# Kernel optimization log

Measured on AMD Instinct MI355X. Metric: run time of the kernel, lower is better.

The kernel has to match this reference:

```python
import jax, jax.numpy as jnp
import numpy as np

NUM_HEADS = 8
KEY_DIM = 512      # total projected dim across heads
VALUE_DIM = 512
EMBED_DIM = 512


def setup_inputs() -> dict:
    key = jax.random.key(0)
    ks = jax.random.split(key, 12)
    B, S, E = 8, 1024, EMBED_DIM
    sc_in = 1.0 / np.sqrt(E)
    sc_o = 1.0 / np.sqrt(KEY_DIM)
    return {
        "queries": jax.random.normal(ks[0], (B, S, E), jnp.float32),
        "keys": jax.random.normal(ks[1], (B, S, E), jnp.float32),
        "values": jax.random.normal(ks[2], (B, S, E), jnp.float32),
        "Wq": jax.random.normal(ks[3], (E, KEY_DIM), jnp.float32) * sc_in,
        "bq": jnp.zeros((KEY_DIM,), jnp.float32),
        "Wk": jax.random.normal(ks[4], (E, KEY_DIM), jnp.float32) * sc_in,
        "bk": jnp.zeros((KEY_DIM,), jnp.float32),
        "Wv": jax.random.normal(ks[5], (E, VALUE_DIM), jnp.float32) * sc_in,
        "bv": jnp.zeros((VALUE_DIM,), jnp.float32),
        "Wo": jax.random.normal(ks[6], (KEY_DIM, EMBED_DIM), jnp.float32) * sc_o,
        "bo": jnp.zeros((EMBED_DIM,), jnp.float32),
    }


def _split_heads(x):
    # [B, S, key_dim] -> [B, H, S, key_dim//H]
    B, S, D = x.shape
    return x.reshape(B, S, NUM_HEADS, D // NUM_HEADS).transpose(0, 2, 1, 3)


def reference(queries, keys, values, Wq, bq, Wk, bk, Wv, bv, Wo, bo):
    q = _split_heads(queries @ Wq + bq)   # [B,H,S,dh]
    k = _split_heads(keys @ Wk + bk)
    v = _split_heads(values @ Wv + bv)
    # NOTE: original scales by sqrt(full key_dim), not per-head dim
    scores = jnp.einsum("bhqd,bhkd->bhqk", q, k) / jnp.sqrt(
        jnp.asarray(KEY_DIM, jnp.float32))
    weights = jax.nn.softmax(scores, axis=-1)
    o = jnp.einsum("bhqk,bhkd->bhqd", weights, v)  # [B,H,S,dh]
    B, H, S, dh = o.shape
    o = o.transpose(0, 2, 1, 3).reshape(B, S, H * dh)  # merge heads -> key_dim
    return o @ Wo + bo
```

## Files before the change

kernel.cpp:

```cpp
#include <hip/hip_runtime.h>


typedef __bf16 bf16x8 __attribute__((ext_vector_type(8)));
typedef __bf16 bf16x4 __attribute__((ext_vector_type(4)));
typedef float  f32x4  __attribute__((ext_vector_type(4)));

#define MFMA(a, b, c) __builtin_amdgcn_mfma_f32_16x16x32_bf16((a), (b), (c), 0, 0, 0)

#define WAITN_BAR(N) asm volatile("s_waitcnt vmcnt(" #N ")\n\ts_barrier" ::: "memory")

__device__ inline float fast_exp2(float x) {
  float r;
  asm("v_exp_f32 %0, %1" : "=v"(r) : "v"(x));
  return r;
}

__device__ inline bf16x8 cvt8(const float* p) {
  f32x4 u = *(const f32x4*)p;
  f32x4 v = *(const f32x4*)(p + 4);
  bf16x8 r;
  r[0] = (__bf16)u[0]; r[1] = (__bf16)u[1]; r[2] = (__bf16)u[2]; r[3] = (__bf16)u[3];
  r[4] = (__bf16)v[0]; r[5] = (__bf16)v[1]; r[6] = (__bf16)v[2]; r[7] = (__bf16)v[3];
  return r;
}

__device__ inline void gl_lds(const __bf16* g, __bf16* l) {
  __builtin_amdgcn_global_load_lds((const __attribute__((address_space(1))) void*)g,
                                   (__attribute__((address_space(3))) void*)l, 16, 0, 0);
}

__global__ __launch_bounds__(256) void prep(
    const float* __restrict__ Q, const float* __restrict__ K,
    const float* __restrict__ V, __bf16* __restrict__ Qo,
    __bf16* __restrict__ Ko, __bf16* __restrict__ Vo,
    const float* __restrict__ W0, const float* __restrict__ W1,
    const float* __restrict__ W2, const float* __restrict__ W3,
    __bf16* __restrict__ O0, __bf16* __restrict__ O1,
    __bf16* __restrict__ O2, __bf16* __restrict__ O3, float s0) {
  const int bx = blockIdx.x;
  if (bx < 2048) {
    const long idx = ((long)bx * 256 + threadIdx.x) * 8;
    *(bf16x8*)(Qo + idx) = cvt8(Q + idx);
    *(bf16x8*)(Ko + idx) = cvt8(K + idx);
    *(bf16x8*)(Vo + idx) = cvt8(V + idx);
    return;
  }
  const int bx2 = bx - 2048;
  const float* in;
  __bf16* out;
  float sc = 1.0f;
  switch (bx2 >> 6) {
    case 0: in = W0; out = O0; sc = s0; break;
    case 1: in = W1; out = O1; break;
    case 2: in = W2; out = O2; break;
    default: in = W3; out = O3; break;
  }
  const int ti = bx2 & 63;
  __shared__ __align__(16) float t[64][65];
  const int tk = (ti & 7) * 64;
  const int tn = (ti >> 3) * 64;
  const int r0 = threadIdx.x >> 4;
  const int c4 = threadIdx.x & 15;
#pragma unroll
  for (int i = 0; i < 4; ++i) {
    int r = r0 + i * 16;
    f32x4 v = *(const f32x4*)(in + (long)(tk + r) * 512 + tn + c4 * 4);
#pragma unroll
    for (int j = 0; j < 4; ++j) t[r][c4 * 4 + j] = v[j] * sc;
  }
  __syncthreads();
  const int n0 = threadIdx.x >> 3;
  const int k8 = threadIdx.x & 7;
#pragma unroll
  for (int i = 0; i < 2; ++i) {
    int n = n0 + i * 32;
    bf16x8 v;
#pragma unroll
    for (int j = 0; j < 8; ++j) v[j] = (__bf16)t[k8 * 8 + j][n];
    *(bf16x8*)(out + (long)(tn + n) * 512 + tk + k8 * 8) = v;
  }
}

template <int MODE, typename OT>
__device__ __forceinline__ void gemm_core(const __bf16* __restrict__ X,
                                          const __bf16* __restrict__ Wt,
                                          const float* __restrict__ bias,
                                          OT* __restrict__ out, float bsc,
                                          char* smem) {
  __bf16* At = (__bf16*)smem;
  __bf16* Bt = (__bf16*)(smem + 24576);

  const int tid = threadIdx.x;
  const int lane = tid & 63, wid = tid >> 6, quad = lane >> 4, l16 = lane & 15;
  const int i = blockIdx.x;
  const int kk = i >> 3;
  const int bm = ((i & 7) * 8 + (kk >> 2)) * 128;
  const int bn = (kk & 3) * 128;
  const int wm = (wid >> 1) * 64;
  const int wn = (wid & 1) * 64;

  f32x4 acc[4][4] = {};

  const int rowB = lane >> 2;
  const int gB = (lane & 3) ^ ((rowB >> 1) & 3);

  auto stage = [&](int off, int k0) {
#pragma unroll
    for (int j = 0; j < 2; ++j) {
      const int g = wid * 2 + j;
      gl_lds(X + (long)(bm + g * 16 + rowB) * 512 + k0 + (gB << 3),
             &At[off + g * 512 + lane * 8]);
      gl_lds(Wt + (long)(bn + g * 16 + rowB) * 512 + k0 + (gB << 3),
             &Bt[off + g * 512 + lane * 8]);
    }
  };

  const int posm = quad ^ ((l16 >> 1) & 3);

  auto compute = [&](int co) {
    bf16x8 a[4], b[4];
#pragma unroll
    for (int t = 0; t < 4; ++t) {
      a[t] = *(const bf16x8*)(&At[co + (wm + t * 16 + l16) * 32 + (posm << 3)]);
      b[t] = *(const bf16x8*)(&Bt[co + (wn + t * 16 + l16) * 32 + (posm << 3)]);
    }
#pragma unroll
    for (int mt = 0; mt < 4; ++mt)
#pragma unroll
      for (int nt = 0; nt < 4; ++nt) acc[mt][nt] = MFMA(a[mt], b[nt], acc[mt][nt]);
  };

  stage(0, 0);
  stage(4096, 32);

  int co = 0, so = 8192;
  for (int c = 0; c < 15; ++c) {
    WAITN_BAR(4);
    if (c < 14) stage(so, (c + 2) * 32);
    compute(co);
    const int nc = 12288 - co - so;
    so = co;
    co = nc;
  }
  WAITN_BAR(0);
  compute(co);

  if constexpr (MODE == 4) {
    __syncthreads();
    __bf16* tb = (__bf16*)smem;
#pragma unroll
    for (int nt = 0; nt < 4; ++nt) {
      const int n = wn + nt * 16 + l16;
      const float bvv = bias[bn + n] * bsc;
#pragma unroll
      for (int mt = 0; mt < 4; ++mt) {
        const int m0 = wm + mt * 16 + quad * 4;
        bf16x4 w;
#pragma unroll
        for (int r = 0; r < 4; ++r) w[r] = (__bf16)(acc[mt][nt][r] + bvv);
        *(bf16x4*)(&tb[n * 128 + (((m0 >> 3) ^ (n & 15)) << 3) + (m0 & 7)]) = w;
      }
    }
    __syncthreads();
    const int nn = tid & 127, mhalf = tid >> 7;
    const int h = (bn + nn) >> 6;
    const int bb = bm >> 10;
    OT* ob = out + (long)(bb * 8 + h) * 65536;
    const int cbase = (bm & 1023) >> 6;
#pragma unroll
    for (int gi = 0; gi < 8; ++gi) {
      const int gl = mhalf * 8 + gi;
      bf16x8 v = *(const bf16x8*)(&tb[nn * 128 + ((gl ^ (nn & 15)) << 3)]);
      const long idx = ((((long)(cbase + (gl >> 3)) * 4 + ((nn >> 4) & 3)) * 2 +
                        ((gl >> 2) & 1)) * 64 + (gl & 3) * 16 + (nn & 15)) * 8;
      *(bf16x8*)(ob + idx) = v;
    }
    return;
  }

#pragma unroll
  for (int nt = 0; nt < 4; ++nt) {
    const int n = bn + wn + nt * 16 + l16;
    const float bvv = bias[n] * bsc;
    const int h = n >> 6, d = n & 63;
#pragma unroll
    for (int mt = 0; mt < 4; ++mt) {
#pragma unroll
      for (int r = 0; r < 4; ++r) {
        const int m = bm + wm + mt * 16 + quad * 4 + r;
        const float v = acc[mt][nt][r] + bvv;
        if constexpr (MODE == 0) {
          out[(long)m * 512 + n] = (OT)v;
        } else if constexpr (MODE == 1) {
          const int bb = m >> 10, s = m & 1023;
          out[((long)((bb * 8 + h) * 1024 + s)) * 64 + d] = (OT)v;
        } else {
          const int bb = m >> 10, s = m & 1023;
          const long idx = (long)(bb * 8 + h) * 65536 +
                           ((((s >> 6) * 4 + ((s >> 4) & 3)) * 2 + (d >> 5)) * 64 +
                            ((d >> 3) & 3) * 16 + (s & 15)) * 8 + (d & 7);
          out[idx] = (OT)v;
        }
      }
    }
  }
}

__global__ __launch_bounds__(256) void gemm_qkv(
    const __bf16* __restrict__ Qx, const __bf16* __restrict__ Kx,
    const __bf16* __restrict__ Vx, const __bf16* __restrict__ Wqt,
    const __bf16* __restrict__ Wkt, const __bf16* __restrict__ Wvt,
    const float* __restrict__ bq, const float* __restrict__ bk,
    const float* __restrict__ bv, __bf16* __restrict__ Qp,
    __bf16* __restrict__ Kp, __bf16* __restrict__ Vtp, float qscale) {
  __shared__ __align__(16) char smem[49152];
  if (blockIdx.y == 0)
    gemm_core<1, __bf16>(Qx, Wqt, bq, Qp, qscale, smem);
  else if (blockIdx.y == 1)
    gemm_core<3, __bf16>(Kx, Wkt, bk, Kp, 1.0f, smem);
  else
    gemm_core<4, __bf16>(Vx, Wvt, bv, Vtp, 1.0f, smem);
}

__global__ __launch_bounds__(256) void gemm_o(const __bf16* __restrict__ Oc,
                                              const __bf16* __restrict__ Wot,
                                              const float* __restrict__ bo,
                                              float* __restrict__ out) {
  __shared__ __align__(16) char smem[49152];
  gemm_core<0, float>(Oc, Wot, bo, out, 1.0f, smem);
}

__global__ __launch_bounds__(256, 2) void attn(const __bf16* __restrict__ Q,
                                               const __bf16* __restrict__ Kf,
                                               const __bf16* __restrict__ Vf,
                                               __bf16* __restrict__ Oc) {
  __shared__ __align__(16) __bf16 plds[4][2048];

  const int tid = threadIdx.x;
  const int lane = tid & 63, wid = tid >> 6, quad = lane >> 4, l16 = lane & 15;
  const int i = blockIdx.x;
  const int pair = (i & 7) + (((i >> 6) & 7) << 3);
  const int qt = (i >> 3) & 7;
  const int q0 = qt * 128 + wid * 32;
  const int b = pair >> 3, h = pair & 7;
  const int swz = l16 & 7;

  const __bf16* Qb = Q + (long)pair * 65536;
  const __bf16* Kb = Kf + (long)pair * 65536 + lane * 8;
  const __bf16* Vb = Vf + (long)pair * 65536 + lane * 8;
  __bf16* pw = plds[wid];

  bf16x8 bq[2][2];
#pragma unroll
  for (int t = 0; t < 2; ++t)
#pragma unroll
    for (int e = 0; e < 2; ++e)
      bq[t][e] = *(const bf16x8*)(Qb + (q0 + t * 16 + l16) * 64 + e * 32 + quad * 8);

  f32x4 lrv[2] = {};
  f32x4 oa[2][4] = {};

#define LOADK(dst, cc)                                                         \
  {                                                                            \
    _Pragma("unroll") for (int kt = 0; kt < 4; ++kt)                           \
        _Pragma("unroll") for (int e = 0; e < 2; ++e)                          \
            dst[kt][e] =                                                       \
        *(const bf16x8*)(Kb + ((((cc) * 4 + kt) * 2 + e) << 9));               \
  }

#define ABODY(kcur, knxt, cc)                                                  \
  {                                                                            \
    bf16x8 vf[4][2];                                                           \
    _Pragma("unroll") for (int nt = 0; nt < 4; ++nt)                           \
        _Pragma("unroll") for (int e = 0; e < 2; ++e)                          \
            vf[nt][e] =                                                        \
        *(const bf16x8*)(Vb + ((((cc) * 4 + nt) * 2 + e) << 9));               \
    f32x4 s[2][4] = {};                                                        \
    __builtin_amdgcn_s_setprio(1);                                             \
    _Pragma("unroll") for (int kt = 0; kt < 4; ++kt)                           \
        _Pragma("unroll") for (int t = 0; t < 2; ++t) {                        \
      s[t][kt] = MFMA(kcur[kt][0], bq[t][0], s[t][kt]);                        \
      s[t][kt] = MFMA(kcur[kt][1], bq[t][1], s[t][kt]);                        \
    }                                                                          \
    __builtin_amdgcn_s_setprio(0);                                             \
    if ((cc) < 15) LOADK(knxt, (cc) + 1);                                      \
    _Pragma("unroll") for (int t = 0; t < 2; ++t) {                            \
      const int prow = (t * 16 + l16) * 64;                                    \
      _Pragma("unroll") for (int kt = 0; kt < 4; ++kt) {                       \
        bf16x4 w;                                                              \
        _Pragma("unroll") for (int r = 0; r < 4; ++r) {                        \
          const float p = fast_exp2(s[t][kt][r]);                              \
          lrv[t][r] += p;                                                      \
          w[r] = (__bf16)p;                                                    \
        }                                                                      \
        *(bf16x4*)(&pw[prow + (((kt * 2 + (quad >> 1)) ^ swz) << 3) +          \
                       (quad & 1) * 4]) = w;                                   \
      }                                                                        \
    }                                                                          \
    bf16x8 pb[2][2];                                                           \
    _Pragma("unroll") for (int t = 0; t < 2; ++t)                              \
        _Pragma("unroll") for (int e = 0; e < 2; ++e)                          \
            pb[t][e] = *(const bf16x8*)(&pw[(t * 16 + l16) * 64 +              \
                                            (((e * 4 + quad) ^ swz) << 3)]);   \
    __builtin_amdgcn_s_setprio(1);                                             \
    _Pragma("unroll") for (int nt = 0; nt < 4; ++nt)                           \
        _Pragma("unroll") for (int t = 0; t < 2; ++t) {                        \
      oa[t][nt] = MFMA(vf[nt][0], pb[t][0], oa[t][nt]);                        \
      oa[t][nt] = MFMA(vf[nt][1], pb[t][1], oa[t][nt]);                        \
    }                                                                          \
    __builtin_amdgcn_s_setprio(0);                                             \
  }

  bf16x8 kA[4][2], kB[4][2];
  LOADK(kA, 0);
#pragma unroll 1
  for (int c = 0; c < 16; c += 2) {
    ABODY(kA, kB, c);
    ABODY(kB, kA, c + 1);
  }
#undef LOADK
#undef ABODY

#pragma unroll
  for (int t = 0; t < 2; ++t) {
    float lr = lrv[t][0] + lrv[t][1] + lrv[t][2] + lrv[t][3];
    lr += __shfl_xor(lr, 16);
    lr += __shfl_xor(lr, 32);
    const float inv = 1.0f / lr;
    const long base = ((long)b * 1024 + q0 + t * 16 + l16) * 512 + h * 64 + quad * 4;
#pragma unroll
    for (int nt = 0; nt < 4; ++nt) {
      bf16x4 w;
#pragma unroll
      for (int r = 0; r < 4; ++r) w[r] = (__bf16)(oa[t][nt][r] * inv);
      *(bf16x4*)(Oc + base + nt * 16) = w;
    }
  }
}

extern "C" void kernel_launch(void* const* d_in, const int* in_sizes, int n_in,
                              void* d_out, int out_size, void* d_ws, size_t ws_size,
                              hipStream_t stream) {
  const float* queries = (const float*)d_in[0];
  const float* keys = (const float*)d_in[1];
  const float* values = (const float*)d_in[2];
  const float* Wq = (const float*)d_in[3];
  const float* bq = (const float*)d_in[4];
  const float* Wk = (const float*)d_in[5];
  const float* bk = (const float*)d_in[6];
  const float* Wv = (const float*)d_in[7];
  const float* bv = (const float*)d_in[8];
  const float* Wo = (const float*)d_in[9];
  const float* bo = (const float*)d_in[10];
  float* out = (float*)d_out;

  __bf16* ws = (__bf16*)d_ws;
  const long WSZ = 512 * 512;
  const long XSZ = 8192L * 512;
  __bf16* Wqt = ws;
  __bf16* Wkt = ws + WSZ;
  __bf16* Wvt = ws + 2 * WSZ;
  __bf16* Wot = ws + 3 * WSZ;
  __bf16* Qp = ws + 4 * WSZ;
  __bf16* Kp = Qp + XSZ;
  __bf16* Vtp = Kp + XSZ;
  __bf16* Oc = Vtp + XSZ;
  __bf16* Qbf = Oc + XSZ;
  __bf16* Kbf = Qbf + XSZ;
  __bf16* Vbf = Kbf + XSZ;

  const float qscale = 0.044194173824159216f * 1.4426950408889634f;

  prep<<<2304, 256, 0, stream>>>(queries, keys, values, Qbf, Kbf, Vbf,
                                 Wq, Wk, Wv, Wo, Wqt, Wkt, Wvt, Wot, qscale);

  gemm_qkv<<<dim3(256, 3), 256, 0, stream>>>(Qbf, Kbf, Vbf, Wqt, Wkt, Wvt,
                                             bq, bk, bv, Qp, Kp, Vtp, qscale);

  attn<<<512, 256, 0, stream>>>(Qp, Kp, Vtp, Oc);

  gemm_o<<<256, 256, 0, stream>>>(Oc, Wot, bo, out);
}
```

Baseline: 161.5 us.

## Pre-swizzle GEMM operands into MFMA fragment layout and load directly to registers

The prep and attention kernels now write activations and transposed weights in a 16-row by 32-column fragment-packed layout, so each lane's bf16x8 operand is contiguous. The GEMM core drops the LDS staging pipeline with its barriers and instead double-buffers fragment loads straight from global memory into registers, with raised MFMA priority. The output GEMM uses a smaller M tile (MT=2) with twice as many blocks, and both GEMMs request 3 waves per SIMD. This removes LDS traffic and synchronisation, but relies on cache and register prefetch to hide global latency, and every producer of the GEMM inputs must follow the new layout.

```diff
diff --git a/kernel.cpp b/kernel.cpp
--- a/kernel.cpp
+++ b/kernel.cpp
@@ -6,8 +6,6 @@
 typedef float  f32x4  __attribute__((ext_vector_type(4)));
 
 #define MFMA(a, b, c) __builtin_amdgcn_mfma_f32_16x16x32_bf16((a), (b), (c), 0, 0, 0)
-
-#define WAITN_BAR(N) asm volatile("s_waitcnt vmcnt(" #N ")\n\ts_barrier" ::: "memory")
 
 __device__ inline float fast_exp2(float x) {
   float r;
@@ -22,11 +20,6 @@
   r[0] = (__bf16)u[0]; r[1] = (__bf16)u[1]; r[2] = (__bf16)u[2]; r[3] = (__bf16)u[3];
   r[4] = (__bf16)v[0]; r[5] = (__bf16)v[1]; r[6] = (__bf16)v[2]; r[7] = (__bf16)v[3];
   return r;
-}
-
-__device__ inline void gl_lds(const __bf16* g, __bf16* l) {
-  __builtin_amdgcn_global_load_lds((const __attribute__((address_space(1))) void*)g,
-                                   (__attribute__((address_space(3))) void*)l, 16, 0, 0);
 }
 
 __global__ __launch_bounds__(256) void prep(
@@ -39,10 +32,13 @@
     __bf16* __restrict__ O2, __bf16* __restrict__ O3, float s0) {
   const int bx = blockIdx.x;
   if (bx < 2048) {
-    const long idx = ((long)bx * 256 + threadIdx.x) * 8;
-    *(bf16x8*)(Qo + idx) = cvt8(Q + idx);
-    *(bf16x8*)(Ko + idx) = cvt8(K + idx);
-    *(bf16x8*)(Vo + idx) = cvt8(V + idx);
+    const long e0 = ((long)bx * 256 + threadIdx.x) * 8;
+    const int m = (int)(e0 >> 9), k = (int)(e0 & 511);
+    const long fa = ((long)((m >> 4) * 16 + (k >> 5))) * 512 +
+                    ((((k >> 3) & 3) * 16 + (m & 15)) << 3);
+    *(bf16x8*)(Qo + fa) = cvt8(Q + e0);
+    *(bf16x8*)(Ko + fa) = cvt8(K + e0);
+    *(bf16x8*)(Vo + fa) = cvt8(V + e0);
     return;
   }
   const int bx2 = bx - 2048;
@@ -73,77 +69,65 @@
   const int k8 = threadIdx.x & 7;
 #pragma unroll
   for (int i = 0; i < 2; ++i) {
-    int n = n0 + i * 32;
+    const int n = tn + n0 + i * 32;
+    const int k = tk + k8 * 8;
     bf16x8 v;
 #pragma unroll
-    for (int j = 0; j < 8; ++j) v[j] = (__bf16)t[k8 * 8 + j][n];
-    *(bf16x8*)(out + (long)(tn + n) * 512 + tk + k8 * 8) = v;
-  }
-}
-
-template <int MODE, typename OT>
+    for (int j = 0; j < 8; ++j) v[j] = (__bf16)t[k8 * 8 + j][n0 + i * 32];
+    const long fa = ((long)((n >> 4) * 16 + (k >> 5))) * 512 +
+                    ((((k >> 3) & 3) * 16 + (n & 15)) << 3);
+    *(bf16x8*)(out + fa) = v;
+  }
+}
+
+template <int MODE, int MT, typename OT>
 __device__ __forceinline__ void gemm_core(const __bf16* __restrict__ X,
                                           const __bf16* __restrict__ Wt,
                                           const float* __restrict__ bias,
                                           OT* __restrict__ out, float bsc,
                                           char* smem) {
-  __bf16* At = (__bf16*)smem;
-  __bf16* Bt = (__bf16*)(smem + 24576);
-
+  constexpr int TM = MT * 32;
+  constexpr int MPX = 8192 / TM / 8;
   const int tid = threadIdx.x;
   const int lane = tid & 63, wid = tid >> 6, quad = lane >> 4, l16 = lane & 15;
   const int i = blockIdx.x;
   const int kk = i >> 3;
-  const int bm = ((i & 7) * 8 + (kk >> 2)) * 128;
+  const int bm = ((i & 7) * MPX + (kk >> 2)) * TM;
   const int bn = (kk & 3) * 128;
-  const int wm = (wid >> 1) * 64;
+  const int wm = (wid >> 1) * (MT * 16);
   const int wn = (wid & 1) * 64;
 
-  f32x4 acc[4][4] = {};
-
-  const int rowB = lane >> 2;
-  const int gB = (lane & 3) ^ ((rowB >> 1) & 3);
-
-  auto stage = [&](int off, int k0) {
-#pragma unroll
-    for (int j = 0; j < 2; ++j) {
-      const int g = wid * 2 + j;
-      gl_lds(X + (long)(bm + g * 16 + rowB) * 512 + k0 + (gB << 3),
-             &At[off + g * 512 + lane * 8]);
-      gl_lds(Wt + (long)(bn + g * 16 + rowB) * 512 + k0 + (gB << 3),
-             &Bt[off + g * 512 + lane * 8]);
-    }
+  const __bf16* Xf = X + (long)((bm + wm) >> 4) * 16 * 512 + lane * 8;
+  const __bf16* Wf = Wt + (long)((bn + wn) >> 4) * 16 * 512 + lane * 8;
+
+  f32x4 acc[MT][4] = {};
+
+  auto loadab = [&](bf16x8 (&a)[MT], bf16x8 (&b)[4], int cc) {
+#pragma unroll
+    for (int t = 0; t < MT; ++t)
+      a[t] = *(const bf16x8*)(Xf + (long)(t * 16 + cc) * 512);
+#pragma unroll
+    for (int t = 0; t < 4; ++t)
+      b[t] = *(const bf16x8*)(Wf + (long)(t * 16 + cc) * 512);
   };
-
-  const int posm = quad ^ ((l16 >> 1) & 3);
-
-  auto compute = [&](int co) {
-    bf16x8 a[4], b[4];
-#pragma unroll
-    for (int t = 0; t < 4; ++t) {
-      a[t] = *(const bf16x8*)(&At[co + (wm + t * 16 + l16) * 32 + (posm << 3)]);
-      b[t] = *(const bf16x8*)(&Bt[co + (wn + t * 16 + l16) * 32 + (posm << 3)]);
-    }
-#pragma unroll
-    for (int mt = 0; mt < 4; ++mt)
+  auto mfmaall = [&](const bf16x8 (&a)[MT], const bf16x8 (&b)[4]) {
+    __builtin_amdgcn_s_setprio(1);
+#pragma unroll
+    for (int mt = 0; mt < MT; ++mt)
 #pragma unroll
       for (int nt = 0; nt < 4; ++nt) acc[mt][nt] = MFMA(a[mt], b[nt], acc[mt][nt]);
+    __builtin_amdgcn_s_setprio(0);
   };
 
-  stage(0, 0);
-  stage(4096, 32);
-
-  int co = 0, so = 8192;
-  for (int c = 0; c < 15; ++c) {
-    WAITN_BAR(4);
-    if (c < 14) stage(so, (c + 2) * 32);
-    compute(co);
-    const int nc = 12288 - co - so;
-    so = co;
-    co = nc;
-  }
-  WAITN_BAR(0);
-  compute(co);
+  bf16x8 aA[MT], bA[4], aB[MT], bB[4];
+  loadab(aA, bA, 0);
+#pragma unroll 1
+  for (int c = 0; c < 16; c += 2) {
+    loadab(aB, bB, c + 1);
+    mfmaall(aA, bA);
+    if (c < 14) loadab(aA, bA, c + 2);
+    mfmaall(aB, bB);
+  }
 
   if constexpr (MODE == 4) {
     __syncthreads();
@@ -184,7 +168,7 @@
     const float bvv = bias[n] * bsc;
     const int h = n >> 6, d = n & 63;
 #pragma unroll
-    for (int mt = 0; mt < 4; ++mt) {
+    for (int mt = 0; mt < MT; ++mt) {
 #pragma unroll
       for (int r = 0; r < 4; ++r) {
         const int m = bm + wm + mt * 16 + quad * 4 + r;
@@ -206,28 +190,27 @@
   }
 }
 
-__global__ __launch_bounds__(256) void gemm_qkv(
+__global__ __launch_bounds__(256, 3) void gemm_qkv(
     const __bf16* __restrict__ Qx, const __bf16* __restrict__ Kx,
     const __bf16* __restrict__ Vx, const __bf16* __restrict__ Wqt,
     const __bf16* __restrict__ Wkt, const __bf16* __restrict__ Wvt,
     const float* __restrict__ bq, const float* __restrict__ bk,
     const float* __restrict__ bv, __bf16* __restrict__ Qp,
     __bf16* __restrict__ Kp, __bf16* __restrict__ Vtp, float qscale) {
-  __shared__ __align__(16) char smem[49152];
+  __shared__ __align__(16) char smem[32768];
   if (blockIdx.y == 0)
-    gemm_core<1, __bf16>(Qx, Wqt, bq, Qp, qscale, smem);
+    gemm_core<1, 4, __bf16>(Qx, Wqt, bq, Qp, qscale, smem);
   else if (blockIdx.y == 1)
-    gemm_core<3, __bf16>(Kx, Wkt, bk, Kp, 1.0f, smem);
+    gemm_core<3, 4, __bf16>(Kx, Wkt, bk, Kp, 1.0f, smem);
   else
-    gemm_core<4, __bf16>(Vx, Wvt, bv, Vtp, 1.0f, smem);
-}
-
-__global__ __launch_bounds__(256) void gemm_o(const __bf16* __restrict__ Oc,
-                                              const __bf16* __restrict__ Wot,
-                                              const float* __restrict__ bo,
-                                              float* __restrict__ out) {
-  __shared__ __align__(16) char smem[49152];
-  gemm_core<0, float>(Oc, Wot, bo, out, 1.0f, smem);
+    gemm_core<4, 4, __bf16>(Vx, Wvt, bv, Vtp, 1.0f, smem);
+}
+
+__global__ __launch_bounds__(256, 3) void gemm_o(const __bf16* __restrict__ Oc,
+                                                 const __bf16* __restrict__ Wot,
+                                                 const float* __restrict__ bo,
+                                                 float* __restrict__ out) {
+  gemm_core<0, 2, float>(Oc, Wot, bo, out, 1.0f, nullptr);
 }
 
 __global__ __launch_bounds__(256, 2) void attn(const __bf16* __restrict__ Q,
@@ -327,13 +310,16 @@
     lr += __shfl_xor(lr, 16);
     lr += __shfl_xor(lr, 32);
     const float inv = 1.0f / lr;
-    const long base = ((long)b * 1024 + q0 + t * 16 + l16) * 512 + h * 64 + quad * 4;
+    const int mrow = b * 1024 + q0 + t * 16;
 #pragma unroll
     for (int nt = 0; nt < 4; ++nt) {
       bf16x4 w;
 #pragma unroll
       for (int r = 0; r < 4; ++r) w[r] = (__bf16)(oa[t][nt][r] * inv);
-      *(bf16x4*)(Oc + base + nt * 16) = w;
+      const int n = h * 64 + nt * 16 + quad * 4;
+      const long fa = ((long)((mrow >> 4) * 16 + (n >> 5))) * 512 +
+                      ((((n >> 3) & 3) * 16 + l16) << 3) + (n & 7);
+      *(bf16x4*)(Oc + fa) = w;
     }
   }
 }
@@ -379,5 +365,5 @@
 
   attn<<<512, 256, 0, stream>>>(Qp, Kp, Vtp, Oc);
 
-  gemm_o<<<256, 256, 0, stream>>>(Oc, Wot, bo, out);
-}
+  gemm_o<<<512, 256, 0, stream>>>(Oc, Wot, bo, out);
+}
```

Measured after the change: 170.9 us. 5.8% more time.

## Enlarge GEMM block tile to 256x128 with per-wave 128x64 output

Applied to the files above, without the earlier changes.

Doubles the M dimension of the projection GEMM tiles so each block computes 256x128 and each wave 128x64 (8x4 MFMA accumulators). This raises arithmetic intensity per LDS load and halves the grid, moving to dynamic shared memory (72KB) with triple-buffered A/B staging and two blocks per CU. The V-transpose epilogue is split per half-tile. The risk is fewer blocks (384 and 128) on a 256-CU device, which leaves many CUs idle, plus higher register pressure from the larger accumulator array.

```diff
diff --git a/kernel.cpp b/kernel.cpp
--- a/kernel.cpp
+++ b/kernel.cpp
@@ -88,73 +88,80 @@
                                           OT* __restrict__ out, float bsc,
                                           char* smem) {
   __bf16* At = (__bf16*)smem;
-  __bf16* Bt = (__bf16*)(smem + 24576);
+  __bf16* Bt = (__bf16*)(smem + 49152);
 
   const int tid = threadIdx.x;
   const int lane = tid & 63, wid = tid >> 6, quad = lane >> 4, l16 = lane & 15;
   const int i = blockIdx.x;
   const int kk = i >> 3;
-  const int bm = ((i & 7) * 8 + (kk >> 2)) * 128;
+  const int bm = ((i & 7) * 4 + (kk >> 2)) * 256;
   const int bn = (kk & 3) * 128;
-  const int wm = (wid >> 1) * 64;
+  const int wm = (wid >> 1) * 128;
   const int wn = (wid & 1) * 64;
 
-  f32x4 acc[4][4] = {};
+  f32x4 acc[8][4] = {};
 
   const int rowB = lane >> 2;
   const int gB = (lane & 3) ^ ((rowB >> 1) & 3);
 
-  auto stage = [&](int off, int k0) {
+  auto stage = [&](int oa, int ob, int k0) {
+#pragma unroll
+    for (int j = 0; j < 4; ++j) {
+      const int g = wid * 4 + j;
+      gl_lds(X + (long)(bm + g * 16 + rowB) * 512 + k0 + (gB << 3),
+             &At[oa + g * 512 + lane * 8]);
+    }
 #pragma unroll
     for (int j = 0; j < 2; ++j) {
       const int g = wid * 2 + j;
-      gl_lds(X + (long)(bm + g * 16 + rowB) * 512 + k0 + (gB << 3),
-             &At[off + g * 512 + lane * 8]);
       gl_lds(Wt + (long)(bn + g * 16 + rowB) * 512 + k0 + (gB << 3),
-             &Bt[off + g * 512 + lane * 8]);
+             &Bt[ob + g * 512 + lane * 8]);
     }
   };
 
   const int posm = quad ^ ((l16 >> 1) & 3);
 
-  auto compute = [&](int co) {
-    bf16x8 a[4], b[4];
-#pragma unroll
-    for (int t = 0; t < 4; ++t) {
-      a[t] = *(const bf16x8*)(&At[co + (wm + t * 16 + l16) * 32 + (posm << 3)]);
-      b[t] = *(const bf16x8*)(&Bt[co + (wn + t * 16 + l16) * 32 + (posm << 3)]);
-    }
-#pragma unroll
-    for (int mt = 0; mt < 4; ++mt)
+  auto compute = [&](int oa, int ob) {
+    bf16x8 a[8], b[4];
+#pragma unroll
+    for (int t = 0; t < 8; ++t)
+      a[t] = *(const bf16x8*)(&At[oa + (wm + t * 16 + l16) * 32 + (posm << 3)]);
+#pragma unroll
+    for (int t = 0; t < 4; ++t)
+      b[t] = *(const bf16x8*)(&Bt[ob + (wn + t * 16 + l16) * 32 + (posm << 3)]);
+#pragma unroll
+    for (int mt = 0; mt < 8; ++mt)
 #pragma unroll
       for (int nt = 0; nt < 4; ++nt) acc[mt][nt] = MFMA(a[mt], b[nt], acc[mt][nt]);
   };
 
-  stage(0, 0);
-  stage(4096, 32);
-
-  int co = 0, so = 8192;
+  stage(0, 0, 0);
+  stage(8192, 4096, 32);
+
+  int coA = 0, soA = 16384, coB = 0, soB = 8192;
   for (int c = 0; c < 15; ++c) {
-    WAITN_BAR(4);
-    if (c < 14) stage(so, (c + 2) * 32);
-    compute(co);
-    const int nc = 12288 - co - so;
-    so = co;
-    co = nc;
+    WAITN_BAR(6);
+    if (c < 14) stage(soA, soB, (c + 2) * 32);
+    compute(coA, coB);
+    const int nA = 24576 - coA - soA;
+    soA = coA; coA = nA;
+    const int nB = 12288 - coB - soB;
+    soB = coB; coB = nB;
   }
   WAITN_BAR(0);
-  compute(co);
+  compute(coA, coB);
 
   if constexpr (MODE == 4) {
     __syncthreads();
-    __bf16* tb = (__bf16*)smem;
+    const int half = wid >> 1;
+    __bf16* tb = (__bf16*)smem + half * 16384;
 #pragma unroll
     for (int nt = 0; nt < 4; ++nt) {
       const int n = wn + nt * 16 + l16;
       const float bvv = bias[bn + n] * bsc;
 #pragma unroll
-      for (int mt = 0; mt < 4; ++mt) {
-        const int m0 = wm + mt * 16 + quad * 4;
+      for (int mt = 0; mt < 8; ++mt) {
+        const int m0 = mt * 16 + quad * 4;
         bf16x4 w;
 #pragma unroll
         for (int r = 0; r < 4; ++r) w[r] = (__bf16)(acc[mt][nt][r] + bvv);
@@ -162,18 +169,18 @@
       }
     }
     __syncthreads();
-    const int nn = tid & 127, mhalf = tid >> 7;
+    const int nn = tid & 127;
     const int h = (bn + nn) >> 6;
     const int bb = bm >> 10;
-    OT* ob = out + (long)(bb * 8 + h) * 65536;
-    const int cbase = (bm & 1023) >> 6;
-#pragma unroll
-    for (int gi = 0; gi < 8; ++gi) {
-      const int gl = mhalf * 8 + gi;
+    OT* ob2 = out + (long)(bb * 8 + h) * 65536;
+    const int mbase = (bm & 1023) + half * 128;
+    const int cbase = mbase >> 6;
+#pragma unroll
+    for (int gl = 0; gl < 16; ++gl) {
       bf16x8 v = *(const bf16x8*)(&tb[nn * 128 + ((gl ^ (nn & 15)) << 3)]);
       const long idx = ((((long)(cbase + (gl >> 3)) * 4 + ((nn >> 4) & 3)) * 2 +
                         ((gl >> 2) & 1)) * 64 + (gl & 3) * 16 + (nn & 15)) * 8;
-      *(bf16x8*)(ob + idx) = v;
+      *(bf16x8*)(ob2 + idx) = v;
     }
     return;
   }
@@ -184,7 +191,7 @@
     const float bvv = bias[n] * bsc;
     const int h = n >> 6, d = n & 63;
 #pragma unroll
-    for (int mt = 0; mt < 4; ++mt) {
+    for (int mt = 0; mt < 8; ++mt) {
 #pragma unroll
       for (int r = 0; r < 4; ++r) {
         const int m = bm + wm + mt * 16 + quad * 4 + r;
@@ -206,14 +213,14 @@
   }
 }
 
-__global__ __launch_bounds__(256) void gemm_qkv(
+__global__ __launch_bounds__(256, 2) void gemm_qkv(
     const __bf16* __restrict__ Qx, const __bf16* __restrict__ Kx,
     const __bf16* __restrict__ Vx, const __bf16* __restrict__ Wqt,
     const __bf16* __restrict__ Wkt, const __bf16* __restrict__ Wvt,
     const float* __restrict__ bq, const float* __restrict__ bk,
     const float* __restrict__ bv, __bf16* __restrict__ Qp,
     __bf16* __restrict__ Kp, __bf16* __restrict__ Vtp, float qscale) {
-  __shared__ __align__(16) char smem[49152];
+  extern __shared__ __align__(16) char smem[];
   if (blockIdx.y == 0)
     gemm_core<1, __bf16>(Qx, Wqt, bq, Qp, qscale, smem);
   else if (blockIdx.y == 1)
@@ -222,11 +229,11 @@
     gemm_core<4, __bf16>(Vx, Wvt, bv, Vtp, 1.0f, smem);
 }
 
-__global__ __launch_bounds__(256) void gemm_o(const __bf16* __restrict__ Oc,
-                                              const __bf16* __restrict__ Wot,
-                                              const float* __restrict__ bo,
-                                              float* __restrict__ out) {
-  __shared__ __align__(16) char smem[49152];
+__global__ __launch_bounds__(256, 2) void gemm_o(const __bf16* __restrict__ Oc,
+                                                 const __bf16* __restrict__ Wot,
+                                                 const float* __restrict__ bo,
+                                                 float* __restrict__ out) {
+  extern __shared__ __align__(16) char smem[];
   gemm_core<0, float>(Oc, Wot, bo, out, 1.0f, smem);
 }
 
@@ -374,10 +381,10 @@
   prep<<<2304, 256, 0, stream>>>(queries, keys, values, Qbf, Kbf, Vbf,
                                  Wq, Wk, Wv, Wo, Wqt, Wkt, Wvt, Wot, qscale);
 
-  gemm_qkv<<<dim3(256, 3), 256, 0, stream>>>(Qbf, Kbf, Vbf, Wqt, Wkt, Wvt,
-                                             bq, bk, bv, Qp, Kp, Vtp, qscale);
+  gemm_qkv<<<dim3(128, 3), 256, 73728, stream>>>(Qbf, Kbf, Vbf, Wqt, Wkt, Wvt,
+                                                 bq, bk, bv, Qp, Kp, Vtp, qscale);
 
   attn<<<512, 256, 0, stream>>>(Qp, Kp, Vtp, Oc);
 
-  gemm_o<<<256, 256, 0, stream>>>(Oc, Wot, bo, out);
-}
+  gemm_o<<<128, 256, 73728, stream>>>(Oc, Wot, bo, out);
+}
```

Measured after the change: 163.8 us. No clear change (+1.4%).
